# Kernel optimization log

Hardware: AMD Instinct MI355X
Metric: run time of the kernel (lower is better)

Reference implementation:

```python
import jax, jax.numpy as jnp
import numpy as np

QMAX = 7.0  # 4-bit symmetric: levels in [-8, 7]

def quant4(w):
    # per-tensor symmetric 4-bit fake-quant with straight-through estimator
    s = jnp.max(jnp.abs(w)) / QMAX
    q = jnp.clip(jnp.round(w / s), -8.0, 7.0) * s
    return w + jax.lax.stop_gradient(q - w)

def setup_inputs() -> dict:
    key = jax.random.key(0)
    ks = jax.random.split(key, 7)
    B = 2048
    x = jax.random.normal(ks[0], (B, 1, 31, 16, 31), dtype=jnp.float32)
    # conv: out_ch=1, in_ch=1, kernel (5,3,5)
    w_conv = jax.random.normal(ks[1], (1, 1, 5, 3, 5), dtype=jnp.float32) * 0.1
    b_conv = jax.random.normal(ks[2], (1,), dtype=jnp.float32) * 0.1
    w_fc1 = jax.random.normal(ks[3], (128, 343), dtype=jnp.float32) * 0.05
    b_fc1 = jax.random.normal(ks[4], (128,), dtype=jnp.float32) * 0.05
    w_fc2 = jax.random.normal(ks[5], (4, 128), dtype=jnp.float32) * 0.05
    b_fc2 = jax.random.normal(ks[6], (4,), dtype=jnp.float32) * 0.05
    return {"x": x, "w_conv": w_conv, "b_conv": b_conv,
            "w_fc1": w_fc1, "b_fc1": b_fc1, "w_fc2": w_fc2, "b_fc2": b_fc2}

def reference(x, w_conv, b_conv, w_fc1, b_fc1, w_fc2, b_fc2):
    # QuantConv3d: 4-bit quantized weights, stride (2,1,2), no padding
    c1 = jax.lax.conv_general_dilated(
        x, quant4(w_conv), window_strides=(2, 1, 2), padding='VALID',
        dimension_numbers=('NCDHW', 'OIDHW', 'NCDHW'))
    c1 = c1 + b_conv.reshape(1, -1, 1, 1, 1)          # [B,1,14,14,14]
    # MaxPool3d(2)
    p1 = jax.lax.reduce_window(c1, -jnp.inf, jax.lax.max,
                               (1, 1, 2, 2, 2), (1, 1, 2, 2, 2), 'VALID')  # [B,1,7,7,7]
    f = p1.reshape(p1.shape[0], -1)                   # [B,343]
    a1 = jax.nn.relu(f @ quant4(w_fc1).T + b_fc1)     # [B,128]
    s2 = a1 @ quant4(w_fc2).T + b_fc2                 # [B,4]
    return jax.nn.softmax(s2, axis=1)
```

## Files before the change

### kernel.cpp

```cpp
#include <hip/hip_runtime.h>
#include <hip/hip_bf16.h>

#define WS_WCONV   128
#define WS_W1B     256
#define WS_W2      44288

__device__ __forceinline__ float q4(float w, float s) {
  if (s <= 0.f) return 0.f;
  float r = rintf(w / s);
  r = fminf(fmaxf(r, -8.f), 7.f);
  return r * s;
}

__global__ __launch_bounds__(256) void quant_all(
    const float* __restrict__ wconv, const float* __restrict__ w1,
    const float* __restrict__ w2, float* __restrict__ ws) {
  __shared__ float red[256];
  int b = blockIdx.x, t = threadIdx.x;
  if (b < 88) {
    const float4* w4 = (const float4*)w1;
    float m = 0.f;
    for (int i = t; i < 10976; i += 256) {
      float4 v = w4[i];
      m = fmaxf(m, fmaxf(fmaxf(fabsf(v.x), fabsf(v.y)),
                         fmaxf(fabsf(v.z), fabsf(v.w))));
    }
    red[t] = m;
    __syncthreads();
    for (int s = 128; s > 0; s >>= 1) {
      if (t < s) red[t] = fmaxf(red[t], red[t + s]);
      __syncthreads();
    }
    float s = red[0] * (1.0f / 7.0f);
    #pragma unroll
    for (int k = 0; k < 2; ++k) {
      int idx = b * 512 + k * 256 + t;
      if (idx < 43904) {
        float q = q4(w1[idx], s);
        int o = idx / 343;
        int j = idx - o * 343;
        ws[WS_W1B + (j >> 2) * 512 + 4 * o + (j & 3)] = q;
      }
    }
  } else {
    float mc = (t < 75) ? fabsf(wconv[t]) : 0.f;
    float m2 = 0.f;
    for (int i = t; i < 512; i += 256) m2 = fmaxf(m2, fabsf(w2[i]));
    red[t] = mc;
    __syncthreads();
    for (int s = 128; s > 0; s >>= 1) {
      if (t < s) red[t] = fmaxf(red[t], red[t + s]);
      __syncthreads();
    }
    float sc = red[0] * (1.0f / 7.0f);
    __syncthreads();
    red[t] = m2;
    __syncthreads();
    for (int s = 128; s > 0; s >>= 1) {
      if (t < s) red[t] = fmaxf(red[t], red[t + s]);
      __syncthreads();
    }
    float s2 = red[0] * (1.0f / 7.0f);
    if (t < 75) ws[WS_WCONV + t] = q4(wconv[t], sc);
    #pragma unroll
    for (int k = 0; k < 2; ++k) {
      int idx = k * 256 + t;
      ws[WS_W2 + idx] = q4(w2[idx], s2);
    }
  }
}

__device__ __forceinline__ void stage(
    const float* __restrict__ x, int b, int d0, int ndep,
    float* __restrict__ xs, int t) {
  const float4* src = (const float4*)(x + (size_t)b * 15376 + d0 * 496);
  float4* dst = (float4*)xs;
  int n = ndep * 124;
  for (int i = t; i < n; i += 256) dst[i] = src[i];
}

__device__ __forceinline__ void conv_phase(
    const float* __restrict__ xs, const float* __restrict__ wq,
    int t, int npf, int pd_off, float bc, float* __restrict__ feat) {
  if (t >= npf) return;
  int pdl = t / 49;
  int rr  = t - pdl * 49;
  int ph  = rr / 7;
  int pw  = rr - ph * 7;
  float c[2][2][2];
  #pragma unroll
  for (int i = 0; i < 8; ++i) ((float*)c)[i] = 0.f;
  int base0 = pdl * 1984 + ph * 62 + pw * 4;
  #pragma unroll
  for (int dd = 0; dd < 7; ++dd) {
    int rbase = base0 + dd * 496;
    #pragma unroll
    for (int hh = 0; hh < 4; ++hh) {
      float row[7];
      #pragma unroll
      for (int wi = 0; wi < 7; ++wi) row[wi] = xs[rbase + hh * 31 + wi];
      #pragma unroll
      for (int odp = 0; odp < 2; ++odp) {
        int kd = dd - 2 * odp;
        if (kd < 0 || kd > 4) continue;
        #pragma unroll
        for (int ohp = 0; ohp < 2; ++ohp) {
          int kh = hh - ohp;
          if (kh < 0 || kh > 2) continue;
          #pragma unroll
          for (int owp = 0; owp < 2; ++owp) {
            float a = c[odp][ohp][owp];
            #pragma unroll
            for (int kw = 0; kw < 5; ++kw)
              a = fmaf(row[2 * owp + kw], wq[kd * 15 + kh * 5 + kw], a);
            c[odp][ohp][owp] = a;
          }
        }
      }
    }
  }
  float m = ((float*)c)[0];
  #pragma unroll
  for (int i = 1; i < 8; ++i) m = fmaxf(m, ((float*)c)[i]);
  feat[(pdl + pd_off) * 49 + rr] = m + bc;
}

__global__ __launch_bounds__(256, 6) void fused_net(
    const float* __restrict__ x, const float* __restrict__ bconv,
    const float* __restrict__ ws, const float* __restrict__ bfc1,
    const float* __restrict__ bfc2, float* __restrict__ out) {
  __shared__ float xs[5456];
  __shared__ float feat[344];
  float* fc1p = xs;
  float* a1   = xs + 128;
  float* s2   = xs + 256;
  int t = threadIdx.x;
  int b = blockIdx.x;
  const float* wq = ws + WS_WCONV;
  float bc = bconv[0];

  if (t == 0) feat[343] = 0.f;
  int par = b & 1;
  #pragma unroll
  for (int ci = 0; ci < 4; ++ci) {
    int c = par ? (3 - ci) : ci;
    int d0 = 8 * c;
    int ndep = (c == 3) ? 7 : 11;
    stage(x, b, d0, ndep, xs, t);
    __syncthreads();
    conv_phase(xs, wq, t, (c == 3) ? 49 : 98, 2 * c, bc, feat);
    __syncthreads();
  }

  int g = t >> 7, o = t & 127;
  {
    const float* w1b = ws + WS_W1B;
    int q0 = g ? 43 : 0;
    const float4* f4 = (const float4*)feat;
    float p0 = 0.f, p1 = 0.f, p2 = 0.f, p3 = 0.f;
    for (int q = q0; q < q0 + 43; ++q) {
      float4 f = f4[q];
      float4 w = *(const float4*)&w1b[q * 512 + 4 * o];
      p0 = fmaf(f.x, w.x, p0);
      p1 = fmaf(f.y, w.y, p1);
      p2 = fmaf(f.z, w.z, p2);
      p3 = fmaf(f.w, w.w, p3);
    }
    float acc = (p0 + p1) + (p2 + p3);
    if (g) fc1p[o] = acc;
    __syncthreads();
    if (!g) a1[o] = fmaxf(acc + fc1p[o] + bfc1[o], 0.f);
  }
  __syncthreads();

  if (t < 64) {
    int cls = t & 3, kk = t >> 2;
    const float4* w2 = (const float4*)(ws + WS_W2 + cls * 128 + kk * 8);
    const float4* av = (const float4*)(a1 + kk * 8);
    float4 aa = av[0], ab = av[1], wa = w2[0], wb = w2[1];
    float p = 0.f;
    p = fmaf(aa.x, wa.x, p); p = fmaf(aa.y, wa.y, p);
    p = fmaf(aa.z, wa.z, p); p = fmaf(aa.w, wa.w, p);
    p = fmaf(ab.x, wb.x, p); p = fmaf(ab.y, wb.y, p);
    p = fmaf(ab.z, wb.z, p); p = fmaf(ab.w, wb.w, p);
    p += __shfl_down(p, 32);
    p += __shfl_down(p, 16);
    p += __shfl_down(p, 8);
    p += __shfl_down(p, 4);
    if (t < 4) s2[t] = p + bfc2[t];
  }
  __syncthreads();
  if (t < 4) {
    float v0 = s2[0], v1 = s2[1], v2 = s2[2], v3 = s2[3];
    float m = fmaxf(fmaxf(v0, v1), fmaxf(v2, v3));
    float e0 = expf(v0 - m), e1 = expf(v1 - m);
    float e2 = expf(v2 - m), e3 = expf(v3 - m);
    float inv = 1.f / (e0 + e1 + e2 + e3);
    float mine = (t == 0) ? e0 : (t == 1) ? e1 : (t == 2) ? e2 : e3;
    out[b * 4 + t] = mine * inv;
  }
}

extern "C" void kernel_launch(void* const* d_in, const int* in_sizes, int n_in,
                              void* d_out, int out_size, void* d_ws, size_t ws_size,
                              hipStream_t stream) {
  const float* x     = (const float*)d_in[0];
  const float* wconv = (const float*)d_in[1];
  const float* bconv = (const float*)d_in[2];
  const float* wfc1  = (const float*)d_in[3];
  const float* bfc1  = (const float*)d_in[4];
  const float* wfc2  = (const float*)d_in[5];
  const float* bfc2  = (const float*)d_in[6];
  float* out = (float*)d_out;
  float* ws  = (float*)d_ws;

  quant_all<<<89, 256, 0, stream>>>(wconv, wfc1, wfc2, ws);
  fused_net<<<2048, 256, 0, stream>>>(x, bconv, ws, bfc1, bfc2, out);
}
```

Before: 230.3 us.

## Stage input in two halves with register prefetch of second half

Replaces the four small depth-chunk stage/conv phases with two larger phases. The first 19 depth slices go into an enlarged shared buffer, and the second half is prefetched into registers while the first half is convolved. This cuts the number of barriers and global-load waits and overlaps the second load with compute. In exchange it uses more LDS and registers, so the occupancy target drops from 6 to 4 blocks per CU. The alternating chunk order by block parity is also dropped.

```diff
diff --git a/kernel.cpp b/kernel.cpp
--- a/kernel.cpp
+++ b/kernel.cpp
@@ -68,15 +68,6 @@
       ws[WS_W2 + idx] = q4(w2[idx], s2);
     }
   }
-}
-
-__device__ __forceinline__ void stage(
-    const float* __restrict__ x, int b, int d0, int ndep,
-    float* __restrict__ xs, int t) {
-  const float4* src = (const float4*)(x + (size_t)b * 15376 + d0 * 496);
-  float4* dst = (float4*)xs;
-  int n = ndep * 124;
-  for (int i = t; i < n; i += 256) dst[i] = src[i];
 }
 
 __device__ __forceinline__ void conv_phase(
@@ -125,11 +116,11 @@
   feat[(pdl + pd_off) * 49 + rr] = m + bc;
 }
 
-__global__ __launch_bounds__(256, 6) void fused_net(
+__global__ __launch_bounds__(256, 4) void fused_net(
     const float* __restrict__ x, const float* __restrict__ bconv,
     const float* __restrict__ ws, const float* __restrict__ bfc1,
     const float* __restrict__ bfc2, float* __restrict__ out) {
-  __shared__ float xs[5456];
+  __shared__ float xs[9424];
   __shared__ float feat[344];
   float* fc1p = xs;
   float* a1   = xs + 128;
@@ -139,18 +130,35 @@
   const float* wq = ws + WS_WCONV;
   float bc = bconv[0];
 
-  if (t == 0) feat[343] = 0.f;
-  int par = b & 1;
-  #pragma unroll
-  for (int ci = 0; ci < 4; ++ci) {
-    int c = par ? (3 - ci) : ci;
-    int d0 = 8 * c;
-    int ndep = (c == 3) ? 7 : 11;
-    stage(x, b, d0, ndep, xs, t);
-    __syncthreads();
-    conv_phase(xs, wq, t, (c == 3) ? 49 : 98, 2 * c, bc, feat);
-    __syncthreads();
-  }
+  {
+    const float4* src = (const float4*)(x + (size_t)b * 15376);
+    float4* dst = (float4*)xs;
+    for (int i = t; i < 2356; i += 256) dst[i] = src[i];
+    if (t == 0) feat[343] = 0.f;
+  }
+  __syncthreads();
+
+  float4 pb[8];
+  {
+    const float4* srcB = (const float4*)(x + (size_t)b * 15376 + 16 * 496);
+    #pragma unroll
+    for (int k = 0; k < 7; ++k) pb[k] = srcB[k * 256 + t];
+    pb[7] = (t < 68) ? srcB[1792 + t] : make_float4(0.f, 0.f, 0.f, 0.f);
+  }
+
+  conv_phase(xs, wq, t, 196, 0, bc, feat);
+  __syncthreads();
+
+  {
+    float4* dst = (float4*)xs;
+    #pragma unroll
+    for (int k = 0; k < 7; ++k) dst[k * 256 + t] = pb[k];
+    if (t < 68) dst[1792 + t] = pb[7];
+  }
+  __syncthreads();
+
+  conv_phase(xs, wq, t, 147, 4, bc, feat);
+  __syncthreads();
 
   int g = t >> 7, o = t & 127;
   {
```

New measurement: 236.5 us. 2.7% more time.
